# Performance work log

Measured on AMD Instinct MI355X. Metric: run time of the kernel, lower is better.

## Reference

```python
import jax, jax.numpy as jnp
import numpy as np

B, N, E = 8, 1024, 512
H, D = 8, 64
F = 2048


def setup_inputs() -> dict:
    key = jax.random.key(0)
    ks = jax.random.split(key, 12)
    s = lambda *sh: 1.0 / np.sqrt(sh[-1])
    inp = {
        "input1": jax.random.normal(ks[0], (B, N, E), dtype=jnp.float32),
        # projection weights stored as [in, out] (torch weight transposed)
        "Wq": jax.random.normal(ks[1], (E, H * D), dtype=jnp.float32) * s(E, E),
        "Wk": jax.random.normal(ks[2], (E, H * D), dtype=jnp.float32) * s(E, E),
        "Wv": jax.random.normal(ks[3], (E, H * D), dtype=jnp.float32) * s(E, E),
        "Wo": jax.random.normal(ks[4], (H * D, E), dtype=jnp.float32) * s(E, E),
        "bo": jnp.zeros((E,), dtype=jnp.float32),
        "g1": jnp.ones((E,), dtype=jnp.float32),
        "b1": jnp.zeros((E,), dtype=jnp.float32),
        "W1": jax.random.normal(ks[5], (E, F), dtype=jnp.float32) * s(E, E),
        "bf1": jnp.zeros((F,), dtype=jnp.float32),
        "W2": jax.random.normal(ks[6], (F, E), dtype=jnp.float32) * s(F, F),
        "bf2": jnp.zeros((E,), dtype=jnp.float32),
        "g2": jnp.ones((E,), dtype=jnp.float32),
        "b2": jnp.zeros((E,), dtype=jnp.float32),
    }
    return inp


def _layernorm(x, g, b, eps=1e-5):
    mu = jnp.mean(x, axis=-1, keepdims=True)
    var = jnp.var(x, axis=-1, keepdims=True)
    return (x - mu) * jax.lax.rsqrt(var + eps) * g + b


def reference(input1, Wq, Wk, Wv, Wo, bo, g1, b1, W1, bf1, W2, bf2, g2, b2):
    x = input1
    # QKV projections, split heads: [B, H, N, D]
    q = (x @ Wq).reshape(B, N, H, D).transpose(0, 2, 1, 3)
    k = (x @ Wk).reshape(B, N, H, D).transpose(0, 2, 1, 3)
    v = (x @ Wv).reshape(B, N, H, D).transpose(0, 2, 1, 3)
    # scaled dot-product attention (naive, materialized scores as in source)
    score = jnp.einsum("bhnd,bhmd->bhnm", q, k) / jnp.sqrt(jnp.float32(D))
    weights = jax.nn.softmax(score, axis=-1)
    out = jnp.einsum("bhnm,bhmd->bhnd", weights, v)
    out_concat = out.transpose(0, 2, 1, 3).reshape(B, N, H * D)
    mh = out_concat @ Wo + bo
    out1 = _layernorm(x + mh, g1, b1)
    ff = jax.nn.relu(out1 @ W1 + bf1) @ W2 + bf2
    out3 = _layernorm(out1 + ff, g2, b2)
    return (out3, 0)
```

## Files before the change

### kernel.cpp

```cpp
#include <hip/hip_runtime.h>
#include <cstdint>
#include <cstddef>

typedef _Float16 h8 __attribute__((ext_vector_type(8)));
typedef _Float16 h4 __attribute__((ext_vector_type(4)));
typedef float    f32x4 __attribute__((ext_vector_type(4)));

constexpr int B_ = 8, N_ = 1024, E_ = 512, H_ = 8, D_ = 64, F_ = 2048;
constexpr int M_ = B_ * N_;
constexpr int HD_ = H_ * D_;

#define QSCALE2 0.18033688011112042f

#define GLOAD_LDS16(gp, lp)                                                        \
    __builtin_amdgcn_global_load_lds((const __attribute__((address_space(1))) void*)(gp), \
                                     (__attribute__((address_space(3))) void*)(lp), 16, 0, 0)

__global__ void __launch_bounds__(256) k_cvt(const float* __restrict__ in,
                                             _Float16* __restrict__ out, int n) {
    int i = (blockIdx.x * 256 + threadIdx.x) * 4;
    if (i + 3 < n) {
        float4 v = *(const float4*)(in + i);
        h4 o = {(_Float16)v.x, (_Float16)v.y, (_Float16)v.z, (_Float16)v.w};
        *(h4*)(out + i) = o;
    }
}

__global__ void __launch_bounds__(256) k_tr6(
    const float* __restrict__ Wq, const float* __restrict__ Wk,
    const float* __restrict__ Wv, const float* __restrict__ Wo,
    const float* __restrict__ W1, const float* __restrict__ W2,
    _Float16* __restrict__ oqkv, _Float16* __restrict__ oo,
    _Float16* __restrict__ o1, _Float16* __restrict__ o2) {
    const float* in;
    _Float16* out;
    int R, C, gt = blockIdx.x;
    switch (blockIdx.z) {
        case 0: in = Wq; out = oqkv;              R = 512;  C = 512;  break;
        case 1: in = Wk; out = oqkv + 512 * 512;  R = 512;  C = 512;  break;
        case 2: in = Wv; out = oqkv + 1024 * 512; R = 512;  C = 512;  break;
        case 3: in = Wo; out = oo;                R = 512;  C = 512;  break;
        default:
            if (blockIdx.z < 8) { in = W1; out = o1; R = 512;  C = 2048; gt += (blockIdx.z - 4) * 256; }
            else                { in = W2; out = o2; R = 2048; C = 512;  gt += (blockIdx.z - 8) * 256; }
    }
    const int ctiles = C >> 5;
    const int ty = gt / ctiles, tx = gt - ty * ctiles;
    const int r0 = ty * 32, c0 = tx * 32;
    __shared__ float lt[32][33];
    const int rr = threadIdx.x >> 3, cq = threadIdx.x & 7;
    float4 v = *(const float4*)&in[(size_t)(r0 + rr) * C + c0 + cq * 4];
    lt[rr][cq * 4 + 0] = v.x; lt[rr][cq * 4 + 1] = v.y;
    lt[rr][cq * 4 + 2] = v.z; lt[rr][cq * 4 + 3] = v.w;
    __syncthreads();
    h4 o = {(_Float16)lt[cq * 4 + 0][rr], (_Float16)lt[cq * 4 + 1][rr],
            (_Float16)lt[cq * 4 + 2][rr], (_Float16)lt[cq * 4 + 3][rr]};
    *(h4*)&out[(size_t)(c0 + rr) * R + r0 + cq * 4] = o;
}

template <int BN, int EPI>
__global__ void __launch_bounds__(256) k_gemm(
    const _Float16* __restrict__ A, const _Float16* __restrict__ Bt,
    int Mg, int Ng, int Kg,
    const float* __restrict__ bias, const float* __restrict__ res,
    float* __restrict__ outf, _Float16* __restrict__ outh,
    _Float16* __restrict__ qp, _Float16* __restrict__ kp, _Float16* __restrict__ vtp) {
    constexpr int WN = BN / 2;
    constexpr int NI = WN / 16;
    __shared__ alignas(16) _Float16 lA[2][64 * 64];
    __shared__ alignas(16) _Float16 lB[2][BN * 64];

    const int tid = threadIdx.x;
    const int lane = tid & 63;
    const int wid = tid >> 6;
    const int wr = wid >> 1, wc = wid & 1;
    const int r16 = lane & 15, hseg = lane >> 4;

    const int bid = blockIdx.x;
    const int xcd = bid & 7;
    const int rem = bid >> 3;
    const int tx = rem >> 4, tyl = rem & 15;
    const int m0 = (xcd * 16 + tyl) * 64;
    const int n0 = tx * BN;

    auto STAGE = [&](int buf, int k0) {
#pragma unroll
        for (int i = 0; i < 2; ++i) {
            const int slot = i * 256 + tid, row = slot >> 3;
            const int cs = (slot & 7) ^ (row & 7);
            GLOAD_LDS16(A + (size_t)(m0 + row) * Kg + k0 + cs * 8, &lA[buf][slot * 8]);
        }
#pragma unroll
        for (int i = 0; i < BN / 32; ++i) {
            const int slot = i * 256 + tid, row = slot >> 3;
            const int cs = (slot & 7) ^ (row & 7);
            GLOAD_LDS16(Bt + (size_t)(n0 + row) * Kg + k0 + cs * 8, &lB[buf][slot * 8]);
        }
    };

    f32x4 acc[2][NI] = {};
    const int nt = Kg >> 6;

    STAGE(0, 0);
    __syncthreads();

    for (int t = 0; t < nt; ++t) {
        const int cur = t & 1;
        if (t + 1 < nt) STAGE(cur ^ 1, (t + 1) << 6);

#pragma unroll
        for (int kk = 0; kk < 2; ++kk) {
            h8 af[2], bf[NI];
#pragma unroll
            for (int mi = 0; mi < 2; ++mi) {
                const int row = wr * 32 + mi * 16 + r16;
                af[mi] = *(const h8*)&lA[cur][row * 64 + (((kk * 4 + hseg) ^ (row & 7)) * 8)];
            }
#pragma unroll
            for (int ni = 0; ni < NI; ++ni) {
                const int row = wc * WN + ni * 16 + r16;
                bf[ni] = *(const h8*)&lB[cur][row * 64 + (((kk * 4 + hseg) ^ (row & 7)) * 8)];
            }
#pragma unroll
            for (int mi = 0; mi < 2; ++mi)
#pragma unroll
                for (int ni = 0; ni < NI; ++ni)
                    acc[mi][ni] =
                        __builtin_amdgcn_mfma_f32_16x16x32_f16(af[mi], bf[ni], acc[mi][ni], 0, 0, 0);
        }
        __syncthreads();
    }

    if constexpr (EPI == 0) {
        if (n0 >= 1024) {
            _Float16* lC = &lA[0][0];
#pragma unroll
            for (int mi = 0; mi < 2; ++mi) {
                const int r0 = wr * 32 + mi * 16 + hseg * 4;
                const int s = r0 >> 3, ro = r0 & 7;
#pragma unroll
                for (int ni = 0; ni < NI; ++ni) {
                    const int c = wc * WN + ni * 16 + r16;
                    h4 pv = {(_Float16)acc[mi][ni][0], (_Float16)acc[mi][ni][1],
                             (_Float16)acc[mi][ni][2], (_Float16)acc[mi][ni][3]};
                    *(h4*)&lC[c * 64 + ((s ^ (c & 7)) << 3) + ro] = pv;
                }
            }
            __syncthreads();
            const int c = tid >> 1, half = tid & 1;
            const int b = m0 >> 10, nn0 = m0 & 1023;
            _Float16* gdst =
                vtp + ((size_t)(b * 512 + (n0 - 1024) + c)) * 1024 + nn0 + half * 32;
#pragma unroll
            for (int j = 0; j < 4; ++j) {
                const int s = half * 4 + j;
                h8 v = *(const h8*)&lC[c * 64 + ((s ^ (c & 7)) << 3)];
                *(h8*)&gdst[j * 8] = v;
            }
        } else {
#pragma unroll
            for (int mi = 0; mi < 2; ++mi)
#pragma unroll
                for (int ni = 0; ni < NI; ++ni)
#pragma unroll
                    for (int r = 0; r < 4; ++r) {
                        int row = m0 + wr * 32 + mi * 16 + hseg * 4 + r;
                        int col = n0 + wc * WN + ni * 16 + r16;
                        float v = acc[mi][ni][r];
                        int cc = col & 511;
                        int h = cc >> 6, d = cc & 63;
                        int b = row >> 10, nn = row & 1023;
                        if (col < 512)
                            qp[((b * 8 + h) * 1024 + nn) * 64 + d] = (_Float16)(v * QSCALE2);
                        else
                            kp[((b * 8 + h) * 1024 + nn) * 64 + d] = (_Float16)v;
                    }
        }
    } else {
#pragma unroll
        for (int mi = 0; mi < 2; ++mi)
#pragma unroll
            for (int ni = 0; ni < NI; ++ni)
#pragma unroll
                for (int r = 0; r < 4; ++r) {
                    int row = m0 + wr * 32 + mi * 16 + hseg * 4 + r;
                    int col = n0 + wc * WN + ni * 16 + r16;
                    float v = acc[mi][ni][r];
                    if constexpr (EPI == 1) {
                        outf[(size_t)row * Ng + col] = v + bias[col] + res[(size_t)row * Ng + col];
                    } else {
                        float t = v + bias[col];
                        outh[(size_t)row * Ng + col] = (_Float16)(t > 0.f ? t : 0.f);
                    }
                }
    }
}

__global__ void __launch_bounds__(256) k_attn(const _Float16* __restrict__ q,
                                              const _Float16* __restrict__ k,
                                              const _Float16* __restrict__ vt,
                                              _Float16* __restrict__ attn) {
    __shared__ alignas(16) _Float16 lK[2][64 * 64];
    __shared__ alignas(16) _Float16 lV[2][64 * 64];
    __shared__ alignas(16) _Float16 lP[4][16 * 64];

    const int tid = threadIdx.x, lane = tid & 63, w = tid >> 6;
    const int bid = blockIdx.x;
    const int xcd = bid & 7, rem = bid >> 3;
    const int bh = xcd * 8 + (rem & 7);
    const int q0 = (rem >> 3) * 64;
    const int r16 = lane & 15, hseg = lane >> 4;
    const size_t base = (size_t)bh * N_ * D_;

    h8 qf[2];
#pragma unroll
    for (int kc = 0; kc < 2; ++kc)
        qf[kc] = *(const h8*)&q[base + (size_t)(q0 + w * 16 + r16) * 64 + kc * 32 + hseg * 8];

    int srow[2], scsrc[2];
#pragma unroll
    for (int i = 0; i < 2; ++i) {
        int slot = i * 256 + tid;
        srow[i] = slot >> 3;
        scsrc[i] = (slot & 7) ^ (srow[i] & 7);
    }

    auto STAGE = [&](int buf, int kt) {
#pragma unroll
        for (int i = 0; i < 2; ++i)
            GLOAD_LDS16(k + base + kt * 4096 + srow[i] * 64 + scsrc[i] * 8,
                        &lK[buf][(i * 256 + tid) * 8]);
#pragma unroll
        for (int i = 0; i < 2; ++i)
            GLOAD_LDS16(vt + base + (size_t)srow[i] * N_ + kt * 64 + scsrc[i] * 8,
                        &lV[buf][(i * 256 + tid) * 8]);
    };

    float mrun = -1e30f, lrun = 0.f;
    f32x4 oacc[4] = {};

    const int pswz = (r16 & 7) * 8;

    STAGE(0, 0);
    __syncthreads();

    for (int kt = 0; kt < N_ / 64; ++kt) {
        const int cur = kt & 1;
        if (kt + 1 < N_ / 64) STAGE(cur ^ 1, kt + 1);

        float sv[4][4];
#pragma unroll
        for (int t4 = 0; t4 < 4; ++t4) {
            f32x4 a = {};
            const int row = t4 * 16 + r16;
#pragma unroll
            for (int kc = 0; kc < 2; ++kc) {
                const int cw = kc * 4 + hseg;
                h8 kf = *(const h8*)&lK[cur][row * 64 + ((cw ^ (row & 7)) * 8)];
                a = __builtin_amdgcn_mfma_f32_16x16x32_f16(kf, qf[kc], a, 0, 0, 0);
            }
#pragma unroll
            for (int r = 0; r < 4; ++r) sv[t4][r] = a[r];
        }

        float mx = sv[0][0];
#pragma unroll
        for (int t4 = 0; t4 < 4; ++t4)
#pragma unroll
            for (int r = 0; r < 4; ++r) mx = fmaxf(mx, sv[t4][r]);
        mx = fmaxf(mx, __shfl_xor(mx, 16));
        mx = fmaxf(mx, __shfl_xor(mx, 32));

        if (__any(mx > mrun + 8.f)) {
            float mnew = fmaxf(mrun, mx);
            float sc = exp2f(mrun - mnew);
            mrun = mnew;
            lrun *= sc;
#pragma unroll
            for (int r = 0; r < 4; ++r) {
                float scq = __shfl(sc, hseg * 4 + r);
#pragma unroll
                for (int nf = 0; nf < 4; ++nf) oacc[nf][r] *= scq;
            }
        }

        float p[4][4];
        float rsum = 0.f;
#pragma unroll
        for (int t4 = 0; t4 < 4; ++t4) {
#pragma unroll
            for (int r = 0; r < 4; ++r) {
                p[t4][r] = exp2f(sv[t4][r] - mrun);
                rsum += p[t4][r];
            }
        }
        rsum += __shfl_xor(rsum, 16);
        rsum += __shfl_xor(rsum, 32);
        lrun += rsum;

#pragma unroll
        for (int t4 = 0; t4 < 4; ++t4) {
            h4 pv = {(_Float16)p[t4][0], (_Float16)p[t4][1],
                     (_Float16)p[t4][2], (_Float16)p[t4][3]};
            *(h4*)&lP[w][r16 * 64 + ((t4 * 16 + hseg * 4) ^ pswz)] = pv;
        }
        asm volatile("s_waitcnt lgkmcnt(0)" ::: "memory");

        h8 pa[2];
#pragma unroll
        for (int kc = 0; kc < 2; ++kc)
            pa[kc] = *(const h8*)&lP[w][r16 * 64 + ((kc * 32 + hseg * 8) ^ pswz)];
#pragma unroll
        for (int nf = 0; nf < 4; ++nf) {
            const int row = nf * 16 + r16;
#pragma unroll
            for (int kc = 0; kc < 2; ++kc) {
                const int cw = kc * 4 + hseg;
                h8 vb = *(const h8*)&lV[cur][row * 64 + ((cw ^ (row & 7)) * 8)];
                oacc[nf] = __builtin_amdgcn_mfma_f32_16x16x32_f16(pa[kc], vb, oacc[nf], 0, 0, 0);
            }
        }
        __syncthreads();
    }

    float rlin = 1.f / lrun;
    int b = bh >> 3, h = bh & 7;
#pragma unroll
    for (int r = 0; r < 4; ++r) {
        float inv = __shfl(rlin, hseg * 4 + r);
        int row = b * 1024 + q0 + w * 16 + hseg * 4 + r;
#pragma unroll
        for (int nf = 0; nf < 4; ++nf) {
            int col = h * 64 + nf * 16 + r16;
            attn[(size_t)row * 512 + col] = (_Float16)(oacc[nf][r] * inv);
        }
    }
}

__global__ void __launch_bounds__(256) k_ln(const float* __restrict__ x,
                                            const float* __restrict__ g,
                                            const float* __restrict__ b,
                                            float* __restrict__ outf,
                                            _Float16* __restrict__ outh,
                                            float* __restrict__ tail) {
    int row = blockIdx.x * 4 + (threadIdx.x >> 6);
    int lane = threadIdx.x & 63;
    const float* xr = x + (size_t)row * 512;
    float4 v0 = *(const float4*)(xr + lane * 8);
    float4 v1 = *(const float4*)(xr + lane * 8 + 4);
    float s = v0.x + v0.y + v0.z + v0.w + v1.x + v1.y + v1.z + v1.w;
    float sq = v0.x * v0.x + v0.y * v0.y + v0.z * v0.z + v0.w * v0.w +
               v1.x * v1.x + v1.y * v1.y + v1.z * v1.z + v1.w * v1.w;
#pragma unroll
    for (int msk = 1; msk < 64; msk <<= 1) {
        s += __shfl_xor(s, msk);
        sq += __shfl_xor(sq, msk);
    }
    float mu = s * (1.f / 512.f);
    float var = sq * (1.f / 512.f) - mu * mu;
    float rstd = rsqrtf(var + 1e-5f);
    float4 ga = *(const float4*)(g + lane * 8);
    float4 gb = *(const float4*)(g + lane * 8 + 4);
    float4 ba = *(const float4*)(b + lane * 8);
    float4 bb = *(const float4*)(b + lane * 8 + 4);
    float o0 = (v0.x - mu) * rstd * ga.x + ba.x;
    float o1 = (v0.y - mu) * rstd * ga.y + ba.y;
    float o2 = (v0.z - mu) * rstd * ga.z + ba.z;
    float o3 = (v0.w - mu) * rstd * ga.w + ba.w;
    float o4 = (v1.x - mu) * rstd * gb.x + bb.x;
    float o5 = (v1.y - mu) * rstd * gb.y + bb.y;
    float o6 = (v1.z - mu) * rstd * gb.z + bb.z;
    float o7 = (v1.w - mu) * rstd * gb.w + bb.w;
    float* orow = outf + (size_t)row * 512 + lane * 8;
    *(float4*)(orow) = make_float4(o0, o1, o2, o3);
    *(float4*)(orow + 4) = make_float4(o4, o5, o6, o7);
    if (outh) {
        h8 oh = {(_Float16)o0, (_Float16)o1, (_Float16)o2, (_Float16)o3,
                 (_Float16)o4, (_Float16)o5, (_Float16)o6, (_Float16)o7};
        *(h8*)(outh + (size_t)row * 512 + lane * 8) = oh;
    }
    if (tail && blockIdx.x == 0 && threadIdx.x == 0) tail[0] = 0.f;
}

extern "C" void kernel_launch(void* const* d_in, const int* in_sizes, int n_in,
                              void* d_out, int out_size, void* d_ws, size_t ws_size,
                              hipStream_t stream) {
    const float* x   = (const float*)d_in[0];
    const float* Wq  = (const float*)d_in[1];
    const float* Wk  = (const float*)d_in[2];
    const float* Wv  = (const float*)d_in[3];
    const float* Wo  = (const float*)d_in[4];
    const float* bo  = (const float*)d_in[5];
    const float* g1  = (const float*)d_in[6];
    const float* b1  = (const float*)d_in[7];
    const float* W1  = (const float*)d_in[8];
    const float* bf1 = (const float*)d_in[9];
    const float* W2  = (const float*)d_in[10];
    const float* bf2 = (const float*)d_in[11];
    const float* g2  = (const float*)d_in[12];
    const float* b2  = (const float*)d_in[13];
    float* out = (float*)d_out;

    char* ws = (char*)d_ws;
    _Float16* xh    = (_Float16*)(ws + 0);
    _Float16* wqkvT = (_Float16*)(ws + 8388608);
    _Float16* woT   = (_Float16*)(ws + 9961472);
    _Float16* w1T   = (_Float16*)(ws + 10485760);
    _Float16* w2T   = (_Float16*)(ws + 12582912);
    _Float16* qb    = (_Float16*)(ws + 14680064);
    _Float16* kb    = (_Float16*)(ws + 23068672);
    _Float16* vtb   = (_Float16*)(ws + 31457280);
    _Float16* attnb = (_Float16*)(ws + 39845888);
    float*    h1    = (float*)(ws + 48234496);
    float*    out1f = (float*)(ws + 65011712);
    _Float16* out1h = xh;
    _Float16* ff    = qb;

    k_cvt<<<dim3(M_ * E_ / 1024), 256, 0, stream>>>(x, xh, M_ * E_);
    k_tr6<<<dim3(256, 1, 12), 256, 0, stream>>>(Wq, Wk, Wv, Wo, W1, W2,
                                                wqkvT, woT, w1T, w2T);

    k_gemm<128, 0><<<dim3(1536), 256, 0, stream>>>(
        xh, wqkvT, M_, 1536, 512, nullptr, nullptr, nullptr, nullptr, qb, kb, vtb);

    k_attn<<<dim3(1024), 256, 0, stream>>>(qb, kb, vtb, attnb);

    k_gemm<64, 1><<<dim3(1024), 256, 0, stream>>>(
        attnb, woT, M_, 512, 512, bo, x, h1, nullptr, nullptr, nullptr, nullptr);

    k_ln<<<dim3(M_ / 4), 256, 0, stream>>>(h1, g1, b1, out1f, out1h, nullptr);

    k_gemm<128, 2><<<dim3(2048), 256, 0, stream>>>(
        out1h, w1T, M_, 2048, 512, bf1, nullptr, nullptr, ff, nullptr, nullptr, nullptr);

    k_gemm<64, 1><<<dim3(1024), 256, 0, stream>>>(
        ff, w2T, M_, 512, 2048, bf2, out1f, h1, nullptr, nullptr, nullptr, nullptr);

    k_ln<<<dim3(M_ / 4), 256, 0, stream>>>(h1, g2, b2, out, nullptr, out + (size_t)M_ * E_);
}
```

Before: 162.4 us.

## Store residual sums in fp16, drop fp32 LN output, restructure attention loop

The GEMM epilogues now write the pre-LayerNorm residual sums as fp16 instead of fp32. The first LayerNorm emits only an fp16 output, which also serves as the residual for the FFN-down GEMM through a new epilogue mode, so the fp32 out1 buffer disappears. This roughly halves the bytes moved between the projection GEMMs and the LayerNorms. The attention kernel is unrolled by two over the double buffers with precomputed swizzled LDS byte offsets and uses packed fp16 conversion for P. The cost is reduced precision in the residual path, including a residual taken from the fp16-rounded LN output rather than fp32.

```diff
diff --git a/kernel.cpp b/kernel.cpp
--- a/kernel.cpp
+++ b/kernel.cpp
@@ -4,6 +4,7 @@
 
 typedef _Float16 h8 __attribute__((ext_vector_type(8)));
 typedef _Float16 h4 __attribute__((ext_vector_type(4)));
+typedef __fp16   g2 __attribute__((ext_vector_type(2)));
 typedef float    f32x4 __attribute__((ext_vector_type(4)));
 
 constexpr int B_ = 8, N_ = 1024, E_ = 512, H_ = 8, D_ = 64, F_ = 2048;
@@ -63,7 +64,7 @@
     const _Float16* __restrict__ A, const _Float16* __restrict__ Bt,
     int Mg, int Ng, int Kg,
     const float* __restrict__ bias, const float* __restrict__ res,
-    float* __restrict__ outf, _Float16* __restrict__ outh,
+    const _Float16* __restrict__ resh, _Float16* __restrict__ outh,
     _Float16* __restrict__ qp, _Float16* __restrict__ kp, _Float16* __restrict__ vtp) {
     constexpr int WN = BN / 2;
     constexpr int NI = WN / 16;
@@ -185,13 +186,15 @@
                 for (int r = 0; r < 4; ++r) {
                     int row = m0 + wr * 32 + mi * 16 + hseg * 4 + r;
                     int col = n0 + wc * WN + ni * 16 + r16;
-                    float v = acc[mi][ni][r];
+                    float v = acc[mi][ni][r] + bias[col];
                     if constexpr (EPI == 1) {
-                        outf[(size_t)row * Ng + col] = v + bias[col] + res[(size_t)row * Ng + col];
+                        v += res[(size_t)row * Ng + col];
+                    } else if constexpr (EPI == 3) {
+                        v += (float)resh[(size_t)row * Ng + col];
                     } else {
-                        float t = v + bias[col];
-                        outh[(size_t)row * Ng + col] = (_Float16)(t > 0.f ? t : 0.f);
+                        v = v > 0.f ? v : 0.f;
                     }
+                    outh[(size_t)row * Ng + col] = (_Float16)v;
                 }
     }
 }
@@ -212,10 +215,8 @@
     const int r16 = lane & 15, hseg = lane >> 4;
     const size_t base = (size_t)bh * N_ * D_;
 
-    h8 qf[2];
-#pragma unroll
-    for (int kc = 0; kc < 2; ++kc)
-        qf[kc] = *(const h8*)&q[base + (size_t)(q0 + w * 16 + r16) * 64 + kc * 32 + hseg * 8];
+    h8 qf0 = *(const h8*)&q[base + (size_t)(q0 + w * 16 + r16) * 64 + hseg * 8];
+    h8 qf1 = *(const h8*)&q[base + (size_t)(q0 + w * 16 + r16) * 64 + 32 + hseg * 8];
 
     int srow[2], scsrc[2];
 #pragma unroll
@@ -239,26 +240,32 @@
     float mrun = -1e30f, lrun = 0.f;
     f32x4 oacc[4] = {};
 
-    const int pswz = (r16 & 7) * 8;
-
-    STAGE(0, 0);
-    __syncthreads();
-
-    for (int kt = 0; kt < N_ / 64; ++kt) {
-        const int cur = kt & 1;
+    const char* lKb = (const char*)&lK[0][0];
+    const char* lVb = (const char*)&lV[0][0];
+    char* lPb = (char*)&lP[0][0] + w * 2048;
+    const int swz = r16 & 7;
+    const int kb0 = r16 * 128 + ((hseg ^ swz) * 16);
+    const int kb1 = r16 * 128 + (((4 + hseg) ^ swz) * 16);
+    const int pswz = swz * 8;
+    const int prd0 = r16 * 128 + (((hseg * 8) ^ pswz) * 2);
+    const int prd1 = r16 * 128 + (((32 + hseg * 8) ^ pswz) * 2);
+    const int pwr0 = r16 * 128 + (((0 + hseg * 4) ^ pswz) * 2);
+    const int pwr1 = r16 * 128 + (((16 + hseg * 4) ^ pswz) * 2);
+    const int pwr2 = r16 * 128 + (((32 + hseg * 4) ^ pswz) * 2);
+    const int pwr3 = r16 * 128 + (((48 + hseg * 4) ^ pswz) * 2);
+
+    auto TILE = [&](const int cur, const int kt) __attribute__((always_inline)) {
         if (kt + 1 < N_ / 64) STAGE(cur ^ 1, kt + 1);
+        const int cOff = cur * 8192;
 
         float sv[4][4];
 #pragma unroll
         for (int t4 = 0; t4 < 4; ++t4) {
             f32x4 a = {};
-            const int row = t4 * 16 + r16;
-#pragma unroll
-            for (int kc = 0; kc < 2; ++kc) {
-                const int cw = kc * 4 + hseg;
-                h8 kf = *(const h8*)&lK[cur][row * 64 + ((cw ^ (row & 7)) * 8)];
-                a = __builtin_amdgcn_mfma_f32_16x16x32_f16(kf, qf[kc], a, 0, 0, 0);
-            }
+            h8 kf0 = *(const h8*)(lKb + cOff + t4 * 2048 + kb0);
+            a = __builtin_amdgcn_mfma_f32_16x16x32_f16(kf0, qf0, a, 0, 0, 0);
+            h8 kf1 = *(const h8*)(lKb + cOff + t4 * 2048 + kb1);
+            a = __builtin_amdgcn_mfma_f32_16x16x32_f16(kf1, qf1, a, 0, 0, 0);
 #pragma unroll
             for (int r = 0; r < 4; ++r) sv[t4][r] = a[r];
         }
@@ -287,40 +294,44 @@
         float p[4][4];
         float rsum = 0.f;
 #pragma unroll
-        for (int t4 = 0; t4 < 4; ++t4) {
+        for (int t4 = 0; t4 < 4; ++t4)
 #pragma unroll
             for (int r = 0; r < 4; ++r) {
                 p[t4][r] = exp2f(sv[t4][r] - mrun);
                 rsum += p[t4][r];
             }
-        }
         rsum += __shfl_xor(rsum, 16);
         rsum += __shfl_xor(rsum, 32);
         lrun += rsum;
 
 #pragma unroll
         for (int t4 = 0; t4 < 4; ++t4) {
-            h4 pv = {(_Float16)p[t4][0], (_Float16)p[t4][1],
-                     (_Float16)p[t4][2], (_Float16)p[t4][3]};
-            *(h4*)&lP[w][r16 * 64 + ((t4 * 16 + hseg * 4) ^ pswz)] = pv;
+            g2 a0 = __builtin_amdgcn_cvt_pkrtz(p[t4][0], p[t4][1]);
+            g2 a1 = __builtin_amdgcn_cvt_pkrtz(p[t4][2], p[t4][3]);
+            h4 pv = {(_Float16)a0[0], (_Float16)a0[1], (_Float16)a1[0], (_Float16)a1[1]};
+            char* dst = lPb + (t4 == 0 ? pwr0 : t4 == 1 ? pwr1 : t4 == 2 ? pwr2 : pwr3);
+            *(h4*)dst = pv;
         }
         asm volatile("s_waitcnt lgkmcnt(0)" ::: "memory");
 
-        h8 pa[2];
-#pragma unroll
-        for (int kc = 0; kc < 2; ++kc)
-            pa[kc] = *(const h8*)&lP[w][r16 * 64 + ((kc * 32 + hseg * 8) ^ pswz)];
+        h8 pa0 = *(const h8*)(lPb + prd0);
+        h8 pa1 = *(const h8*)(lPb + prd1);
 #pragma unroll
         for (int nf = 0; nf < 4; ++nf) {
-            const int row = nf * 16 + r16;
-#pragma unroll
-            for (int kc = 0; kc < 2; ++kc) {
-                const int cw = kc * 4 + hseg;
-                h8 vb = *(const h8*)&lV[cur][row * 64 + ((cw ^ (row & 7)) * 8)];
-                oacc[nf] = __builtin_amdgcn_mfma_f32_16x16x32_f16(pa[kc], vb, oacc[nf], 0, 0, 0);
-            }
+            h8 vb0 = *(const h8*)(lVb + cOff + nf * 2048 + kb0);
+            oacc[nf] = __builtin_amdgcn_mfma_f32_16x16x32_f16(pa0, vb0, oacc[nf], 0, 0, 0);
+            h8 vb1 = *(const h8*)(lVb + cOff + nf * 2048 + kb1);
+            oacc[nf] = __builtin_amdgcn_mfma_f32_16x16x32_f16(pa1, vb1, oacc[nf], 0, 0, 0);
         }
         __syncthreads();
+    };
+
+    STAGE(0, 0);
+    __syncthreads();
+
+    for (int kt = 0; kt < N_ / 64; kt += 2) {
+        TILE(0, kt);
+        TILE(1, kt + 1);
     }
 
     float rlin = 1.f / lrun;
@@ -337,7 +348,8 @@
     }
 }
 
-__global__ void __launch_bounds__(256) k_ln(const float* __restrict__ x,
+template <int OUTF32>
+__global__ void __launch_bounds__(256) k_ln(const _Float16* __restrict__ x,
                                             const float* __restrict__ g,
                                             const float* __restrict__ b,
                                             float* __restrict__ outf,
@@ -345,12 +357,15 @@
                                             float* __restrict__ tail) {
     int row = blockIdx.x * 4 + (threadIdx.x >> 6);
     int lane = threadIdx.x & 63;
-    const float* xr = x + (size_t)row * 512;
-    float4 v0 = *(const float4*)(xr + lane * 8);
-    float4 v1 = *(const float4*)(xr + lane * 8 + 4);
-    float s = v0.x + v0.y + v0.z + v0.w + v1.x + v1.y + v1.z + v1.w;
-    float sq = v0.x * v0.x + v0.y * v0.y + v0.z * v0.z + v0.w * v0.w +
-               v1.x * v1.x + v1.y * v1.y + v1.z * v1.z + v1.w * v1.w;
+    h8 v = *(const h8*)(x + (size_t)row * 512 + lane * 8);
+    float f[8];
+    float s = 0.f, sq = 0.f;
+#pragma unroll
+    for (int j = 0; j < 8; ++j) {
+        f[j] = (float)v[j];
+        s += f[j];
+        sq += f[j] * f[j];
+    }
 #pragma unroll
     for (int msk = 1; msk < 64; msk <<= 1) {
         s += __shfl_xor(s, msk);
@@ -363,23 +378,25 @@
     float4 gb = *(const float4*)(g + lane * 8 + 4);
     float4 ba = *(const float4*)(b + lane * 8);
     float4 bb = *(const float4*)(b + lane * 8 + 4);
-    float o0 = (v0.x - mu) * rstd * ga.x + ba.x;
-    float o1 = (v0.y - mu) * rstd * ga.y + ba.y;
-    float o2 = (v0.z - mu) * rstd * ga.z + ba.z;
-    float o3 = (v0.w - mu) * rstd * ga.w + ba.w;
-    float o4 = (v1.x - mu) * rstd * gb.x + bb.x;
-    float o5 = (v1.y - mu) * rstd * gb.y + bb.y;
-    float o6 = (v1.z - mu) * rstd * gb.z + bb.z;
-    float o7 = (v1.w - mu) * rstd * gb.w + bb.w;
-    float* orow = outf + (size_t)row * 512 + lane * 8;
-    *(float4*)(orow) = make_float4(o0, o1, o2, o3);
-    *(float4*)(orow + 4) = make_float4(o4, o5, o6, o7);
-    if (outh) {
-        h8 oh = {(_Float16)o0, (_Float16)o1, (_Float16)o2, (_Float16)o3,
-                 (_Float16)o4, (_Float16)o5, (_Float16)o6, (_Float16)o7};
+    float o[8];
+    o[0] = (f[0] - mu) * rstd * ga.x + ba.x;
+    o[1] = (f[1] - mu) * rstd * ga.y + ba.y;
+    o[2] = (f[2] - mu) * rstd * ga.z + ba.z;
+    o[3] = (f[3] - mu) * rstd * ga.w + ba.w;
+    o[4] = (f[4] - mu) * rstd * gb.x + bb.x;
+    o[5] = (f[5] - mu) * rstd * gb.y + bb.y;
+    o[6] = (f[6] - mu) * rstd * gb.z + bb.z;
+    o[7] = (f[7] - mu) * rstd * gb.w + bb.w;
+    if constexpr (OUTF32) {
+        float* orow = outf + (size_t)row * 512 + lane * 8;
+        *(float4*)(orow) = make_float4(o[0], o[1], o[2], o[3]);
+        *(float4*)(orow + 4) = make_float4(o[4], o[5], o[6], o[7]);
+        if (tail && blockIdx.x == 0 && threadIdx.x == 0) tail[0] = 0.f;
+    } else {
+        h8 oh = {(_Float16)o[0], (_Float16)o[1], (_Float16)o[2], (_Float16)o[3],
+                 (_Float16)o[4], (_Float16)o[5], (_Float16)o[6], (_Float16)o[7]};
         *(h8*)(outh + (size_t)row * 512 + lane * 8) = oh;
     }
-    if (tail && blockIdx.x == 0 && threadIdx.x == 0) tail[0] = 0.f;
 }
 
 extern "C" void kernel_launch(void* const* d_in, const int* in_sizes, int n_in,
@@ -411,8 +428,7 @@
     _Float16* kb    = (_Float16*)(ws + 23068672);
     _Float16* vtb   = (_Float16*)(ws + 31457280);
     _Float16* attnb = (_Float16*)(ws + 39845888);
-    float*    h1    = (float*)(ws + 48234496);
-    float*    out1f = (float*)(ws + 65011712);
+    _Float16* h1h   = (_Float16*)(ws + 48234496);
     _Float16* out1h = xh;
     _Float16* ff    = qb;
 
@@ -426,15 +442,15 @@
     k_attn<<<dim3(1024), 256, 0, stream>>>(qb, kb, vtb, attnb);
 
     k_gemm<64, 1><<<dim3(1024), 256, 0, stream>>>(
-        attnb, woT, M_, 512, 512, bo, x, h1, nullptr, nullptr, nullptr, nullptr);
-
-    k_ln<<<dim3(M_ / 4), 256, 0, stream>>>(h1, g1, b1, out1f, out1h, nullptr);
+        attnb, woT, M_, 512, 512, bo, x, nullptr, h1h, nullptr, nullptr, nullptr);
+
+    k_ln<0><<<dim3(M_ / 4), 256, 0, stream>>>(h1h, g1, b1, nullptr, out1h, nullptr);
 
     k_gemm<128, 2><<<dim3(2048), 256, 0, stream>>>(
         out1h, w1T, M_, 2048, 512, bf1, nullptr, nullptr, ff, nullptr, nullptr, nullptr);
 
-    k_gemm<64, 1><<<dim3(1024), 256, 0, stream>>>(
-        ff, w2T, M_, 512, 2048, bf2, out1f, h1, nullptr, nullptr, nullptr, nullptr);
-
-    k_ln<<<dim3(M_ / 4), 256, 0, stream>>>(h1, g2, b2, out, nullptr, out + (size_t)M_ * E_);
-}
+    k_gemm<64, 3><<<dim3(1024), 256, 0, stream>>>(
+        ff, w2T, M_, 512, 2048, bf2, nullptr, out1h, h1h, nullptr, nullptr, nullptr);
+
+    k_ln<1><<<dim3(M_ / 4), 256, 0, stream>>>(h1h, g2, b2, out, nullptr, out + (size_t)M_ * E_);
+}
```

Result: faster. 152.2 us (-6.3%).
